# Optimization experiments

Hardware: AMD Instinct MI355X
Metric: run time of the kernel (lower is better)

The kernel has to match this reference:

```python
import jax, jax.numpy as jnp
import numpy as np

NUM_TOKENS = 131072
N_EXPERTS = 256
N_GROUP = 8
TOPK_GROUP = 4
TOP_K = 8
ROUTED_SCALING = 2.5


def setup_inputs() -> dict:
    key = jax.random.key(0)
    k1, k2 = jax.random.split(key)
    router_logits = jax.random.normal(k1, (NUM_TOKENS, N_EXPERTS), dtype=jnp.float32)
    correction_bias = jax.random.normal(k2, (N_EXPERTS,), dtype=jnp.float32) * 0.1
    return {"router_logits": router_logits, "correction_bias": correction_bias}


def reference(router_logits, correction_bias):
    T = router_logits.shape[0]
    eg = N_EXPERTS // N_GROUP  # experts per group = 32

    scores = jax.nn.sigmoid(router_logits).astype(jnp.float32)          # [T, 256]
    scores_for_choice = scores + correction_bias[None, :]                # [T, 256]

    # group score = sum of top-2 corrected scores within each group
    grp = scores_for_choice.reshape(T, N_GROUP, eg)                      # [T, 8, 32]
    top2, _ = jax.lax.top_k(grp, 2)                                      # [T, 8, 2]
    group_scores = top2.sum(axis=-1)                                     # [T, 8]

    # pick top groups, build expert-level mask
    _, group_idx = jax.lax.top_k(group_scores, TOPK_GROUP)               # [T, 4]
    rows = jnp.arange(T)[:, None]
    group_mask = jnp.zeros_like(group_scores).at[rows, group_idx].set(1.0)  # [T, 8]
    score_mask = jnp.repeat(group_mask, eg, axis=-1)                     # [T, 256]

    masked_scores = jnp.where(score_mask > 0, scores_for_choice, 0.0)
    _, topk_indices = jax.lax.top_k(masked_scores, TOP_K)                # [T, 8]

    topk_weights = jnp.take_along_axis(scores, topk_indices, axis=1)     # [T, 8]
    denom = topk_weights.sum(axis=-1, keepdims=True) + 1e-20
    topk_weights = topk_weights / denom * ROUTED_SCALING
    return (topk_indices, topk_weights)
```

## Files before the change

kernel.cpp:

```cpp
#include <hip/hip_runtime.h>
#include <math.h>


constexpr int N_EXPERTS   = 256;
constexpr int N_GROUP     = 8;
constexpr int EG          = 32;
constexpr int TOPK_GROUP  = 4;
constexpr int TOP_K       = 8;

__device__ __forceinline__ void insert8(float (&lv)[8], float (&li)[8], float v, float i) {
#pragma unroll
  for (int k = 0; k < 8; ++k) {
    const bool gt = v > lv[k];
    const float nv = gt ? lv[k] : v;
    const float ni = gt ? li[k] : i;
    lv[k] = gt ? v : lv[k];
    li[k] = gt ? i : li[k];
    v = nv; i = ni;
  }
}

__device__ __forceinline__ bool keyGE(float va, float ia, float vb, float ib) {
  return (va > vb) || (va == vb && ia < ib);
}

__device__ __forceinline__ void takeMax(float va, float ia, float vb, float ib,
                                        float& vo, float& io) {
  const bool a = keyGE(va, ia, vb, ib);
  vo = a ? va : vb;
  io = a ? ia : ib;
}

__device__ __forceinline__ void cswap(float& va, float& ia, float& vb, float& ib) {
  const bool a = keyGE(va, ia, vb, ib);
  const float v1 = a ? va : vb, i1 = a ? ia : ib;
  const float v2 = a ? vb : va, i2 = a ? ib : ia;
  va = v1; ia = i1; vb = v2; ib = i2;
}

__device__ __forceinline__ void merge8(const float (&Av)[8], const float (&Ai)[8],
                                       const float (&Bv)[8], const float (&Bi)[8],
                                       float (&Rv)[8], float (&Ri)[8]) {
#pragma unroll
  for (int i = 0; i < 8; ++i) takeMax(Av[i], Ai[i], Bv[7 - i], Bi[7 - i], Rv[i], Ri[i]);
#pragma unroll
  for (int i = 0; i < 4; ++i) cswap(Rv[i], Ri[i], Rv[i + 4], Ri[i + 4]);
  cswap(Rv[0], Ri[0], Rv[2], Ri[2]);
  cswap(Rv[1], Ri[1], Rv[3], Ri[3]);
  cswap(Rv[4], Ri[4], Rv[6], Ri[6]);
  cswap(Rv[5], Ri[5], Rv[7], Ri[7]);
  cswap(Rv[0], Ri[0], Rv[1], Ri[1]);
  cswap(Rv[2], Ri[2], Rv[3], Ri[3]);
  cswap(Rv[4], Ri[4], Rv[5], Ri[5]);
  cswap(Rv[6], Ri[6], Rv[7], Ri[7]);
}

__global__ __launch_bounds__(256, 2) void deepseek_topk_router(
    const float* __restrict__ logits,
    const float* __restrict__ bias,
    float* __restrict__ out,
    int T) {
  const int t = blockIdx.x * 256 + threadIdx.x;
  if (t >= T) return;

  const float4* row4 = reinterpret_cast<const float4*>(logits + (size_t)t * N_EXPERTS);

  float lv[N_GROUP][8];
  float li[N_GROUP][8];

#pragma unroll
  for (int g = 0; g < N_GROUP; ++g) {
#pragma unroll
    for (int k = 0; k < 8; ++k) { lv[g][k] = -INFINITY; li[g][k] = 0.0f; }
    for (int q = 0; q < 8; ++q) {
      const float4 x = row4[g * 8 + q];
      const float xs[4] = {x.x, x.y, x.z, x.w};
#pragma unroll
      for (int e = 0; e < 4; ++e) {
        const int idx = g * EG + q * 4 + e;
        const float s = 1.0f / (1.0f + expf(-xs[e]));
        const float c = s + bias[idx];
        insert8(lv[g], li[g], c, (float)idx);
      }
    }
  }

  float gs[N_GROUP];
#pragma unroll
  for (int g = 0; g < N_GROUP; ++g) gs[g] = lv[g][0] + lv[g][1];

#pragma unroll
  for (int g = 0; g < N_GROUP; ++g) {
    int rank = 0;
#pragma unroll
    for (int h = 0; h < N_GROUP; ++h)
      rank += ((gs[h] > gs[g]) || (gs[h] == gs[g] && h < g)) ? 1 : 0;
    const bool sel = (rank < TOPK_GROUP);
#pragma unroll
    for (int k = 0; k < 8; ++k) lv[g][k] = sel ? lv[g][k] : 0.0f;
  }

  float m0v[8], m0i[8], m1v[8], m1i[8], m2v[8], m2i[8], m3v[8], m3i[8];
  merge8(lv[0], li[0], lv[1], li[1], m0v, m0i);
  merge8(lv[2], li[2], lv[3], li[3], m1v, m1i);
  merge8(lv[4], li[4], lv[5], li[5], m2v, m2i);
  merge8(lv[6], li[6], lv[7], li[7], m3v, m3i);
  float n0v[8], n0i[8], n1v[8], n1i[8];
  merge8(m0v, m0i, m1v, m1i, n0v, n0i);
  merge8(m2v, m2i, m3v, m3i, n1v, n1i);
  float fv[8], fi[8];
  merge8(n0v, n0i, n1v, n1i, fv, fi);

  float sv[8];
  float sum = 0.0f;
#pragma unroll
  for (int k = 0; k < TOP_K; ++k) {
    const int id = (int)fi[k];
    sv[k] = fv[k] - bias[id];
    sum += sv[k];
  }
  const float denom = sum + 1e-20f;
  const float scale = 2.5f / denom;

  float4* oi = reinterpret_cast<float4*>(out) + (size_t)t * 2;
  oi[0] = make_float4(fi[0], fi[1], fi[2], fi[3]);
  oi[1] = make_float4(fi[4], fi[5], fi[6], fi[7]);
  float4* ow = reinterpret_cast<float4*>(out + (size_t)T * TOP_K) + (size_t)t * 2;
  ow[0] = make_float4(sv[0] * scale, sv[1] * scale, sv[2] * scale, sv[3] * scale);
  ow[1] = make_float4(sv[4] * scale, sv[5] * scale, sv[6] * scale, sv[7] * scale);
}

extern "C" void kernel_launch(void* const* d_in, const int* in_sizes, int n_in,
                              void* d_out, int out_size, void* d_ws, size_t ws_size,
                              hipStream_t stream) {
  const float* logits = (const float*)d_in[0];
  const float* bias   = (const float*)d_in[1];
  float* out = (float*)d_out;
  const int T = in_sizes[0] / N_EXPERTS;
  const int blocks = (T + 255) / 256;
  deepseek_topk_router<<<blocks, 256, 0, stream>>>(logits, bias, out, T);
}
```

Baseline: 250.5 us.

## Split each token across eight threads, one per group, with LDS butterfly merge

Instead of one thread per token walking all 256 experts, each token now gets 8 threads, each handling one 32-expert group. Group ranking is done through a shared-memory exchange of group scores, and the per-group top-8 lists are combined with a 3-stage xor butterfly merge through LDS. The goal is more parallelism and better-coalesced row loads, plus far fewer registers per thread than the old 8x8 list arrays, so occupancy should rise. In exchange it adds block-wide barriers, 16 KB of LDS traffic per merge stage, and redundant merge work on all 8 lanes.

```diff
diff --git a/kernel.cpp b/kernel.cpp
--- a/kernel.cpp
+++ b/kernel.cpp
@@ -7,6 +7,7 @@
 constexpr int EG          = 32;
 constexpr int TOPK_GROUP  = 4;
 constexpr int TOP_K       = 8;
+constexpr int BLOCK       = 256;
 
 __device__ __forceinline__ void insert8(float (&lv)[8], float (&li)[8], float v, float i) {
 #pragma unroll
@@ -55,79 +56,101 @@
   cswap(Rv[6], Ri[6], Rv[7], Ri[7]);
 }
 
-__global__ __launch_bounds__(256, 2) void deepseek_topk_router(
+__global__ __launch_bounds__(256, 2) void deepseek_topk_router_lds(
     const float* __restrict__ logits,
     const float* __restrict__ bias,
     float* __restrict__ out,
     int T) {
-  const int t = blockIdx.x * 256 + threadIdx.x;
-  if (t >= T) return;
+  __shared__ float gsbuf[BLOCK];
+  __shared__ float exv[8 * BLOCK];
+  __shared__ float exi[8 * BLOCK];
 
-  const float4* row4 = reinterpret_cast<const float4*>(logits + (size_t)t * N_EXPERTS);
+  const int tid = threadIdx.x;
+  const int id  = blockIdx.x * BLOCK + tid;
+  const int t   = id >> 3;
+  const int q   = id & 7;
 
-  float lv[N_GROUP][8];
-  float li[N_GROUP][8];
+  const float4* row4 =
+      reinterpret_cast<const float4*>(logits + (size_t)t * N_EXPERTS + q * EG);
+  const float4* b4 = reinterpret_cast<const float4*>(bias + q * EG);
+
+  float lv[8], li[8];
+#pragma unroll
+  for (int k = 0; k < 8; ++k) { lv[k] = -INFINITY; li[k] = 0.0f; }
 
 #pragma unroll
-  for (int g = 0; g < N_GROUP; ++g) {
+  for (int u = 0; u < 8; ++u) {
+    const float4 x = row4[u];
+    const float4 bb = b4[u];
+    const float xs[4] = {x.x, x.y, x.z, x.w};
+    const float bs[4] = {bb.x, bb.y, bb.z, bb.w};
 #pragma unroll
-    for (int k = 0; k < 8; ++k) { lv[g][k] = -INFINITY; li[g][k] = 0.0f; }
-    for (int q = 0; q < 8; ++q) {
-      const float4 x = row4[g * 8 + q];
-      const float xs[4] = {x.x, x.y, x.z, x.w};
-#pragma unroll
-      for (int e = 0; e < 4; ++e) {
-        const int idx = g * EG + q * 4 + e;
-        const float s = 1.0f / (1.0f + expf(-xs[e]));
-        const float c = s + bias[idx];
-        insert8(lv[g], li[g], c, (float)idx);
-      }
+    for (int e = 0; e < 4; ++e) {
+      const int idx = q * EG + u * 4 + e;
+      const float s = 1.0f / (1.0f + expf(-xs[e]));
+      const float c = s + bs[e];
+      insert8(lv, li, c, (float)idx);
     }
   }
 
-  float gs[N_GROUP];
+  const float gs = lv[0] + lv[1];
+  gsbuf[tid] = gs;
+  __syncthreads();
+  const int cbase = tid & ~7;
+  int rank = 0;
 #pragma unroll
-  for (int g = 0; g < N_GROUP; ++g) gs[g] = lv[g][0] + lv[g][1];
+  for (int h = 0; h < N_GROUP; ++h) {
+    const float other = gsbuf[cbase + h];
+    rank += ((other > gs) || (other == gs && h < q)) ? 1 : 0;
+  }
+  const bool sel = (rank < TOPK_GROUP);
+#pragma unroll
+  for (int k = 0; k < 8; ++k) lv[k] = sel ? lv[k] : 0.0f;
 
+  float pv[8], pi[8], rv[8], ri[8];
 #pragma unroll
-  for (int g = 0; g < N_GROUP; ++g) {
-    int rank = 0;
+  for (int d = 1; d <= 4; d <<= 1) {
+    __syncthreads();
 #pragma unroll
-    for (int h = 0; h < N_GROUP; ++h)
-      rank += ((gs[h] > gs[g]) || (gs[h] == gs[g] && h < g)) ? 1 : 0;
-    const bool sel = (rank < TOPK_GROUP);
+    for (int k = 0; k < 8; ++k) {
+      exv[k * BLOCK + tid] = lv[k];
+      exi[k * BLOCK + tid] = li[k];
+    }
+    __syncthreads();
+    const int p = tid ^ d;
 #pragma unroll
-    for (int k = 0; k < 8; ++k) lv[g][k] = sel ? lv[g][k] : 0.0f;
+    for (int k = 0; k < 8; ++k) {
+      pv[k] = exv[k * BLOCK + p];
+      pi[k] = exi[k * BLOCK + p];
+    }
+    merge8(lv, li, pv, pi, rv, ri);
+#pragma unroll
+    for (int k = 0; k < 8; ++k) { lv[k] = rv[k]; li[k] = ri[k]; }
   }
-
-  float m0v[8], m0i[8], m1v[8], m1i[8], m2v[8], m2i[8], m3v[8], m3i[8];
-  merge8(lv[0], li[0], lv[1], li[1], m0v, m0i);
-  merge8(lv[2], li[2], lv[3], li[3], m1v, m1i);
-  merge8(lv[4], li[4], lv[5], li[5], m2v, m2i);
-  merge8(lv[6], li[6], lv[7], li[7], m3v, m3i);
-  float n0v[8], n0i[8], n1v[8], n1i[8];
-  merge8(m0v, m0i, m1v, m1i, n0v, n0i);
-  merge8(m2v, m2i, m3v, m3i, n1v, n1i);
-  float fv[8], fi[8];
-  merge8(n0v, n0i, n1v, n1i, fv, fi);
 
   float sv[8];
   float sum = 0.0f;
 #pragma unroll
   for (int k = 0; k < TOP_K; ++k) {
-    const int id = (int)fi[k];
-    sv[k] = fv[k] - bias[id];
+    const int idf = (int)li[k];
+    sv[k] = lv[k] - bias[idf];
     sum += sv[k];
   }
-  const float denom = sum + 1e-20f;
-  const float scale = 2.5f / denom;
+  const float scale = 2.5f / (sum + 1e-20f);
 
-  float4* oi = reinterpret_cast<float4*>(out) + (size_t)t * 2;
-  oi[0] = make_float4(fi[0], fi[1], fi[2], fi[3]);
-  oi[1] = make_float4(fi[4], fi[5], fi[6], fi[7]);
-  float4* ow = reinterpret_cast<float4*>(out + (size_t)T * TOP_K) + (size_t)t * 2;
-  ow[0] = make_float4(sv[0] * scale, sv[1] * scale, sv[2] * scale, sv[3] * scale);
-  ow[1] = make_float4(sv[4] * scale, sv[5] * scale, sv[6] * scale, sv[7] * scale);
+  if (q < 4) {
+    float4 vout;
+    if (q == 0)      vout = make_float4(li[0], li[1], li[2], li[3]);
+    else if (q == 1) vout = make_float4(li[4], li[5], li[6], li[7]);
+    else if (q == 2) vout = make_float4(sv[0] * scale, sv[1] * scale,
+                                        sv[2] * scale, sv[3] * scale);
+    else             vout = make_float4(sv[4] * scale, sv[5] * scale,
+                                        sv[6] * scale, sv[7] * scale);
+    const size_t half = (q < 2) ? 0 : (size_t)T * TOP_K;
+    const int    sub  = q & 1;
+    float4* dst = reinterpret_cast<float4*>(out + half) + (size_t)t * 2 + sub;
+    *dst = vout;
+  }
 }
 
 extern "C" void kernel_launch(void* const* d_in, const int* in_sizes, int n_in,
@@ -137,6 +160,7 @@
   const float* bias   = (const float*)d_in[1];
   float* out = (float*)d_out;
   const int T = in_sizes[0] / N_EXPERTS;
-  const int blocks = (T + 255) / 256;
-  deepseek_topk_router<<<blocks, 256, 0, stream>>>(logits, bias, out, T);
+  const long threads = (long)T * N_GROUP;
+  const int blocks = (int)((threads + BLOCK - 1) / BLOCK);
+  deepseek_topk_router_lds<<<blocks, BLOCK, 0, stream>>>(logits, bias, out, T);
 }
```

Result: faster. 217.8 us (-13.1%).

## Split each token across eight threads with packed u64 keys and LDS merge

Applied to the files above, without the earlier changes.

Each token's work is now spread over eight threads, one per expert group. Each thread computes a sorted top-8 list of packed 64-bit (monotone value, inverted index) keys using a sorting network and merges. The per-group lists and group scores go through shared memory, and one thread per token picks the top four groups and merges their lists. This is meant to raise parallelism, give coalesced loads, and cut the comparison cost of the serial insertion sort. In exchange, seven eighths of the threads sit idle in the final phase, the kernel uses 32KB+ of LDS per block, and it assumes T is divisible by 64.

```diff
diff --git a/kernel.cpp b/kernel.cpp
--- a/kernel.cpp
+++ b/kernel.cpp
@@ -2,130 +2,159 @@
 #include <math.h>
 
 
-constexpr int N_EXPERTS   = 256;
-constexpr int N_GROUP     = 8;
-constexpr int EG          = 32;
-constexpr int TOPK_GROUP  = 4;
-constexpr int TOP_K       = 8;
+constexpr int N_EXPERTS  = 256;
+constexpr int N_GROUP    = 8;
+constexpr int EG         = 32;
+constexpr int TOPK_GROUP = 4;
+constexpr int TOP_K      = 8;
+constexpr int BLOCK      = 512;
+constexpr int TPB_TOK    = BLOCK / N_GROUP;
 
-__device__ __forceinline__ void insert8(float (&lv)[8], float (&li)[8], float v, float i) {
-#pragma unroll
-  for (int k = 0; k < 8; ++k) {
-    const bool gt = v > lv[k];
-    const float nv = gt ? lv[k] : v;
-    const float ni = gt ? li[k] : i;
-    lv[k] = gt ? v : lv[k];
-    li[k] = gt ? i : li[k];
-    v = nv; i = ni;
-  }
+typedef unsigned int u32;
+typedef unsigned long long u64;
+
+__device__ __forceinline__ u32 fmono(float f) {
+  const u32 u = __float_as_uint(f);
+  return u ^ ((u32)((int)u >> 31) | 0x80000000u);
+}
+__device__ __forceinline__ float fmono_inv(u32 m) {
+  const u32 u = (m & 0x80000000u) ? (m ^ 0x80000000u) : ~m;
+  return __uint_as_float(u);
+}
+__device__ __forceinline__ u64 mkkey(float v, int idx) {
+  return ((u64)fmono(v) << 32) | (u32)(255 - idx);
+}
+__device__ __forceinline__ int key_idx(u64 k) { return 255 - (int)(k & 0xFFu); }
+__device__ __forceinline__ float key_val(u64 k) { return fmono_inv((u32)(k >> 32)); }
+
+__device__ __forceinline__ void kswap(u64& a, u64& b) {
+  const bool sw = b > a;
+  const u64 t = sw ? b : a;
+  b = sw ? a : b;
+  a = t;
 }
 
-__device__ __forceinline__ bool keyGE(float va, float ia, float vb, float ib) {
-  return (va > vb) || (va == vb && ia < ib);
+__device__ __forceinline__ void sort8(u64 (&k)[8]) {
+  kswap(k[0], k[1]); kswap(k[2], k[3]); kswap(k[4], k[5]); kswap(k[6], k[7]);
+  kswap(k[0], k[2]); kswap(k[1], k[3]); kswap(k[4], k[6]); kswap(k[5], k[7]);
+  kswap(k[1], k[2]); kswap(k[5], k[6]);
+  kswap(k[0], k[4]); kswap(k[1], k[5]); kswap(k[2], k[6]); kswap(k[3], k[7]);
+  kswap(k[2], k[4]); kswap(k[3], k[5]);
+  kswap(k[1], k[2]); kswap(k[3], k[4]); kswap(k[5], k[6]);
 }
 
-__device__ __forceinline__ void takeMax(float va, float ia, float vb, float ib,
-                                        float& vo, float& io) {
-  const bool a = keyGE(va, ia, vb, ib);
-  vo = a ? va : vb;
-  io = a ? ia : ib;
+__device__ __forceinline__ void merge8(u64 (&A)[8], const u64 (&B)[8]) {
+  u64 R[8];
+#pragma unroll
+  for (int i = 0; i < 8; ++i) {
+    const bool a = A[i] >= B[7 - i];
+    R[i] = a ? A[i] : B[7 - i];
+  }
+  kswap(R[0], R[4]); kswap(R[1], R[5]); kswap(R[2], R[6]); kswap(R[3], R[7]);
+  kswap(R[0], R[2]); kswap(R[1], R[3]); kswap(R[4], R[6]); kswap(R[5], R[7]);
+  kswap(R[0], R[1]); kswap(R[2], R[3]); kswap(R[4], R[5]); kswap(R[6], R[7]);
+#pragma unroll
+  for (int i = 0; i < 8; ++i) A[i] = R[i];
 }
 
-__device__ __forceinline__ void cswap(float& va, float& ia, float& vb, float& ib) {
-  const bool a = keyGE(va, ia, vb, ib);
-  const float v1 = a ? va : vb, i1 = a ? ia : ib;
-  const float v2 = a ? vb : va, i2 = a ? ib : ia;
-  va = v1; ia = i1; vb = v2; ib = i2;
-}
-
-__device__ __forceinline__ void merge8(const float (&Av)[8], const float (&Ai)[8],
-                                       const float (&Bv)[8], const float (&Bi)[8],
-                                       float (&Rv)[8], float (&Ri)[8]) {
-#pragma unroll
-  for (int i = 0; i < 8; ++i) takeMax(Av[i], Ai[i], Bv[7 - i], Bi[7 - i], Rv[i], Ri[i]);
-#pragma unroll
-  for (int i = 0; i < 4; ++i) cswap(Rv[i], Ri[i], Rv[i + 4], Ri[i + 4]);
-  cswap(Rv[0], Ri[0], Rv[2], Ri[2]);
-  cswap(Rv[1], Ri[1], Rv[3], Ri[3]);
-  cswap(Rv[4], Ri[4], Rv[6], Ri[6]);
-  cswap(Rv[5], Ri[5], Rv[7], Ri[7]);
-  cswap(Rv[0], Ri[0], Rv[1], Ri[1]);
-  cswap(Rv[2], Ri[2], Rv[3], Ri[3]);
-  cswap(Rv[4], Ri[4], Rv[5], Ri[5]);
-  cswap(Rv[6], Ri[6], Rv[7], Ri[7]);
-}
-
-__global__ __launch_bounds__(256, 2) void deepseek_topk_router(
+__global__ __launch_bounds__(BLOCK, 2) void deepseek_topk_router_r7(
     const float* __restrict__ logits,
     const float* __restrict__ bias,
     float* __restrict__ out,
     int T) {
-  const int t = blockIdx.x * 256 + threadIdx.x;
-  if (t >= T) return;
+  __shared__ __align__(16) float gsb[BLOCK];
+  __shared__ u64 kbuf[N_GROUP][BLOCK];
 
-  const float4* row4 = reinterpret_cast<const float4*>(logits + (size_t)t * N_EXPERTS);
+  const int tid = threadIdx.x;
+  const int id  = blockIdx.x * BLOCK + tid;
+  const int t   = id >> 3;
+  const int q   = id & 7;
 
-  float lv[N_GROUP][8];
-  float li[N_GROUP][8];
+  const float4* row4 =
+      reinterpret_cast<const float4*>(logits + (size_t)t * N_EXPERTS + q * EG);
+  const float4* b4 = reinterpret_cast<const float4*>(bias + q * EG);
 
+  u64 K[8];
 #pragma unroll
-  for (int g = 0; g < N_GROUP; ++g) {
+  for (int c = 0; c < 4; ++c) {
+    u64 C[8];
+    const float4 x0 = row4[2 * c], x1 = row4[2 * c + 1];
+    const float4 c0 = b4[2 * c],   c1 = b4[2 * c + 1];
+    const float xs[8] = {x0.x, x0.y, x0.z, x0.w, x1.x, x1.y, x1.z, x1.w};
+    const float bs[8] = {c0.x, c0.y, c0.z, c0.w, c1.x, c1.y, c1.z, c1.w};
 #pragma unroll
-    for (int k = 0; k < 8; ++k) { lv[g][k] = -INFINITY; li[g][k] = 0.0f; }
-    for (int q = 0; q < 8; ++q) {
-      const float4 x = row4[g * 8 + q];
-      const float xs[4] = {x.x, x.y, x.z, x.w};
+    for (int j = 0; j < 8; ++j) {
+      const float e = expf(-xs[j]);
+      const float s = 1.0f / (1.0f + e);
+      C[j] = mkkey(s + bs[j], q * EG + c * 8 + j);
+    }
+    sort8(C);
+    if (c == 0) {
 #pragma unroll
-      for (int e = 0; e < 4; ++e) {
-        const int idx = g * EG + q * 4 + e;
-        const float s = 1.0f / (1.0f + expf(-xs[e]));
-        const float c = s + bias[idx];
-        insert8(lv[g], li[g], c, (float)idx);
-      }
+      for (int j = 0; j < 8; ++j) K[j] = C[j];
+    } else {
+      merge8(K, C);
     }
   }
 
-  float gs[N_GROUP];
+  gsb[tid] = key_val(K[0]) + key_val(K[1]);
 #pragma unroll
-  for (int g = 0; g < N_GROUP; ++g) gs[g] = lv[g][0] + lv[g][1];
+  for (int k = 0; k < 8; ++k) kbuf[k][tid] = K[k];
+  __syncthreads();
+  if (tid >= TPB_TOK) return;
 
+  const int j   = tid;
+  const int tok = blockIdx.x * TPB_TOK + j;
+
+  const float4* gp = reinterpret_cast<const float4*>(&gsb[8 * j]);
+  const float4 ga = gp[0], gb = gp[1];
+  const float g[N_GROUP] = {ga.x, ga.y, ga.z, ga.w, gb.x, gb.y, gb.z, gb.w};
+
+  int s0 = 0, s1 = 0, s2 = 0, s3 = 0, cnt = 0;
 #pragma unroll
-  for (int g = 0; g < N_GROUP; ++g) {
+  for (int h = 0; h < N_GROUP; ++h) {
     int rank = 0;
 #pragma unroll
-    for (int h = 0; h < N_GROUP; ++h)
-      rank += ((gs[h] > gs[g]) || (gs[h] == gs[g] && h < g)) ? 1 : 0;
-    const bool sel = (rank < TOPK_GROUP);
-#pragma unroll
-    for (int k = 0; k < 8; ++k) lv[g][k] = sel ? lv[g][k] : 0.0f;
+    for (int m = 0; m < N_GROUP; ++m)
+      rank += (m < h) ? (g[m] >= g[h] ? 1 : 0) : (g[m] > g[h] ? 1 : 0);
+    const bool pick = (rank < TOPK_GROUP);
+    s0 = (pick && cnt == 0) ? h : s0;
+    s1 = (pick && cnt == 1) ? h : s1;
+    s2 = (pick && cnt == 2) ? h : s2;
+    s3 = (pick && cnt == 3) ? h : s3;
+    cnt += pick ? 1 : 0;
   }
 
-  float m0v[8], m0i[8], m1v[8], m1i[8], m2v[8], m2i[8], m3v[8], m3i[8];
-  merge8(lv[0], li[0], lv[1], li[1], m0v, m0i);
-  merge8(lv[2], li[2], lv[3], li[3], m1v, m1i);
-  merge8(lv[4], li[4], lv[5], li[5], m2v, m2i);
-  merge8(lv[6], li[6], lv[7], li[7], m3v, m3i);
-  float n0v[8], n0i[8], n1v[8], n1i[8];
-  merge8(m0v, m0i, m1v, m1i, n0v, n0i);
-  merge8(m2v, m2i, m3v, m3i, n1v, n1i);
-  float fv[8], fi[8];
-  merge8(n0v, n0i, n1v, n1i, fv, fi);
+  u64 A[8], B[8];
+  const int base = 8 * j;
+#pragma unroll
+  for (int k = 0; k < 8; ++k) A[k] = kbuf[k][base + s0];
+#pragma unroll
+  for (int k = 0; k < 8; ++k) B[k] = kbuf[k][base + s1];
+  merge8(A, B);
+#pragma unroll
+  for (int k = 0; k < 8; ++k) B[k] = kbuf[k][base + s2];
+  merge8(A, B);
+#pragma unroll
+  for (int k = 0; k < 8; ++k) B[k] = kbuf[k][base + s3];
+  merge8(A, B);
 
-  float sv[8];
+  float fi[8], sv[8];
   float sum = 0.0f;
 #pragma unroll
   for (int k = 0; k < TOP_K; ++k) {
-    const int id = (int)fi[k];
-    sv[k] = fv[k] - bias[id];
+    const int idx = key_idx(A[k]);
+    const float c = key_val(A[k]);
+    sv[k] = c - bias[idx];
+    fi[k] = (float)idx;
     sum += sv[k];
   }
-  const float denom = sum + 1e-20f;
-  const float scale = 2.5f / denom;
+  const float scale = 2.5f / (sum + 1e-20f);
 
-  float4* oi = reinterpret_cast<float4*>(out) + (size_t)t * 2;
+  float4* oi = reinterpret_cast<float4*>(out) + (size_t)tok * 2;
   oi[0] = make_float4(fi[0], fi[1], fi[2], fi[3]);
   oi[1] = make_float4(fi[4], fi[5], fi[6], fi[7]);
-  float4* ow = reinterpret_cast<float4*>(out + (size_t)T * TOP_K) + (size_t)t * 2;
+  float4* ow = reinterpret_cast<float4*>(out + (size_t)T * TOP_K) + (size_t)tok * 2;
   ow[0] = make_float4(sv[0] * scale, sv[1] * scale, sv[2] * scale, sv[3] * scale);
   ow[1] = make_float4(sv[4] * scale, sv[5] * scale, sv[6] * scale, sv[7] * scale);
 }
@@ -137,6 +166,6 @@
   const float* bias   = (const float*)d_in[1];
   float* out = (float*)d_out;
   const int T = in_sizes[0] / N_EXPERTS;
-  const int blocks = (T + 255) / 256;
-  deepseek_topk_router<<<blocks, 256, 0, stream>>>(logits, bias, out, T);
+  const int blocks = T / TPB_TOK;
+  deepseek_topk_router_r7<<<blocks, BLOCK, 0, stream>>>(logits, bias, out, T);
 }
```

New measurement: 212.2 us. 15.3% less time.
